# Optimization experiments

Measured on AMD Instinct MI355X. Metric: run time of the kernel, lower is better.

Reference implementation:

```python
import jax, jax.numpy as jnp
import numpy as np

OFFSET_SCALE = 6.0
S = 256
N = S * S  # 65536 UV grid points


def setup_inputs() -> dict:
    key = jax.random.key(0)
    k1, k2, k3, k4 = jax.random.split(key, 4)
    B = 64
    Offset = jax.random.normal(k1, (B, 3, S, S), dtype=jnp.float32)
    Posmap_kpt = jax.random.normal(k2, (B, 3, S, S), dtype=jnp.float32)
    mean_posmap = jax.random.normal(k3, (3, S, S), dtype=jnp.float32)
    uv_kpt = jax.random.randint(k4, (68, 2), 0, S, dtype=jnp.int32)
    return {"Offset": Offset, "Posmap_kpt": Posmap_kpt,
            "mean_posmap": mean_posmap, "uv_kpt": uv_kpt}


def reference(Offset, Posmap_kpt, mean_posmap, uv_kpt):
    B = Offset.shape[0]
    # offsetmap / kptmap: NCHW -> NHWC
    offsetmap = jnp.transpose(Offset * OFFSET_SCALE + mean_posmap[None], (0, 2, 3, 1))  # [B,256,256,3]
    kptmap = jnp.transpose(Posmap_kpt, (0, 2, 3, 1))                                    # [B,256,256,3]

    kpt_dst = kptmap[:, uv_kpt[:, 0], uv_kpt[:, 1]]     # [B,68,3]
    kpt_src = offsetmap[:, uv_kpt[:, 0], uv_kpt[:, 1]]  # [B,68,3]
    offsetflat = offsetmap.reshape(B, N, 3)

    # 16 quadruples of consecutive keypoints: (x, x+1, x+2, x+3) for x in 0,4,...,60
    quad = (jnp.arange(0, 64, 4)[:, None] + jnp.arange(4)[None, :])  # [16,4]
    p = kpt_src[:, quad]  # [B,16,4,3]
    q = kpt_dst[:, quad]  # [B,16,4,3]

    # Batched closed-form rigid fit: A = p0 - p{1,2,3}, Bm = q0 - q{1,2,3}
    A = p[:, :, 0:1, :] - p[:, :, 1:, :]   # [B,16,3,3]
    Bm = q[:, :, 0:1, :] - q[:, :, 1:, :]  # [B,16,3,3]
    R = jnp.linalg.inv(A) @ Bm             # [B,16,3,3]
    T = jnp.mean(q - p @ R, axis=-2)       # [B,16,3]

    # Coarse rotation -> yaw -> keypoint visibility
    R_coarse = jnp.mean(R, axis=1)  # [B,3,3]
    yaw = jnp.arctan2(-R_coarse[:, 2, 0],
                      jnp.sqrt(R_coarse[:, 0, 0] ** 2 + R_coarse[:, 1, 0] ** 2))
    yaw_rate = yaw / jnp.pi
    left = jnp.maximum(yaw_rate * S, 0.0)        # [B]
    right = jnp.minimum(S + yaw_rate * S, float(S))  # [B]
    col = uv_kpt[:, 1].astype(jnp.float32)       # [68]
    vis = jnp.where((col[None, :] <= left[:, None]) | (col[None, :] >= right[:, None]),
                    0.001, 1.0)                  # [B,68]

    # Visibility-weighted average of per-quad transforms
    w = jnp.prod(vis[:, quad], axis=-1)          # [B,16]
    s = jnp.sum(w, axis=1)                       # [B]
    R_p = jnp.einsum('bq,bqij->bij', w, R) / s[:, None, None]  # [B,3,3]
    T_p = jnp.einsum('bq,bqi->bi', w, T) / s[:, None]          # [B,3]

    out = offsetflat @ R_p + T_p[:, None, :]     # [B,65536,3]
    return jnp.transpose(out.reshape(B, S, S, 3), (0, 3, 1, 2))  # [B,3,256,256]
```

## Files before the change

### kernel.cpp

```cpp
#include <hip/hip_runtime.h>
#include <math.h>

#define S 256
#define NPIX (S * S)
#define B 64
#define NQUAD 16

__global__ __launch_bounds__(64) void pose_solve_kernel(
    const float* __restrict__ Offset,
    const float* __restrict__ Posmap,
    const float* __restrict__ meanp,
    const int*   __restrict__ uv,
    float*       __restrict__ params)
{
    const int b = blockIdx.x;
    const int t = threadIdx.x;

    __shared__ double sp[64][3];
    __shared__ double sq[64][3];
    __shared__ double sR[NQUAD][9];
    __shared__ double sT[NQUAD][3];
    __shared__ int    scol[64];

    {
        const int u = uv[2 * t + 0];
        const int v = uv[2 * t + 1];
        scol[t] = v;
        const int n = u * S + v;
        const float* offb = Offset + (size_t)b * 3 * NPIX;
        const float* posb = Posmap + (size_t)b * 3 * NPIX;
#pragma unroll
        for (int c = 0; c < 3; ++c) {
            sp[t][c] = (double)offb[c * NPIX + n] * 6.0 + (double)meanp[c * NPIX + n];
            sq[t][c] = (double)posb[c * NPIX + n];
        }
    }
    __syncthreads();

    if (t < NQUAD) {
        const int k0 = 4 * t;
        double A[3][3], Bm[3][3];
#pragma unroll
        for (int r = 0; r < 3; ++r)
#pragma unroll
            for (int c = 0; c < 3; ++c) {
                A[r][c]  = sp[k0][c] - sp[k0 + 1 + r][c];
                Bm[r][c] = sq[k0][c] - sq[k0 + 1 + r][c];
            }
        const double c00 = A[1][1] * A[2][2] - A[1][2] * A[2][1];
        const double c01 = A[1][2] * A[2][0] - A[1][0] * A[2][2];
        const double c02 = A[1][0] * A[2][1] - A[1][1] * A[2][0];
        const double det = A[0][0] * c00 + A[0][1] * c01 + A[0][2] * c02;
        const double id  = 1.0 / det;
        double inv[3][3];
        inv[0][0] = c00 * id;
        inv[0][1] = (A[0][2] * A[2][1] - A[0][1] * A[2][2]) * id;
        inv[0][2] = (A[0][1] * A[1][2] - A[0][2] * A[1][1]) * id;
        inv[1][0] = c01 * id;
        inv[1][1] = (A[0][0] * A[2][2] - A[0][2] * A[2][0]) * id;
        inv[1][2] = (A[0][2] * A[1][0] - A[0][0] * A[1][2]) * id;
        inv[2][0] = c02 * id;
        inv[2][1] = (A[0][1] * A[2][0] - A[0][0] * A[2][1]) * id;
        inv[2][2] = (A[0][0] * A[1][1] - A[0][1] * A[1][0]) * id;

        double R[3][3];
#pragma unroll
        for (int i = 0; i < 3; ++i)
#pragma unroll
            for (int j = 0; j < 3; ++j) {
                R[i][j] = inv[i][0] * Bm[0][j] + inv[i][1] * Bm[1][j] + inv[i][2] * Bm[2][j];
                sR[t][i * 3 + j] = R[i][j];
            }
#pragma unroll
        for (int c = 0; c < 3; ++c) {
            double acc = 0.0;
#pragma unroll
            for (int j = 0; j < 4; ++j) {
                const double pr = sp[k0 + j][0] * R[0][c] +
                                  sp[k0 + j][1] * R[1][c] +
                                  sp[k0 + j][2] * R[2][c];
                acc += sq[k0 + j][c] - pr;
            }
            sT[t][c] = acc * 0.25;
        }
    }
    __syncthreads();

    if (t == 0) {
        double r00 = 0.0, r10 = 0.0, r20 = 0.0;
        for (int q = 0; q < NQUAD; ++q) {
            r00 += sR[q][0];
            r10 += sR[q][3];
            r20 += sR[q][6];
        }
        r00 /= NQUAD; r10 /= NQUAD; r20 /= NQUAD;
        const double yaw = atan2(-r20, sqrt(r00 * r00 + r10 * r10));
        const double yr  = yaw / M_PI;
        const double left  = fmax(yr * (double)S, 0.0);
        const double right = fmin((double)S + yr * (double)S, (double)S);

        double w[NQUAD];
        double s = 0.0;
        for (int q = 0; q < NQUAD; ++q) {
            double wq = 1.0;
#pragma unroll
            for (int j = 0; j < 4; ++j) {
                const double col = (double)scol[4 * q + j];
                const double vis = (col <= left || col >= right) ? 0.001 : 1.0;
                wq *= vis;
            }
            w[q] = wq;
            s += wq;
        }
        double Rp[9] = {0, 0, 0, 0, 0, 0, 0, 0, 0};
        double Tp[3] = {0, 0, 0};
        for (int q = 0; q < NQUAD; ++q) {
#pragma unroll
            for (int e = 0; e < 9; ++e) Rp[e] += w[q] * sR[q][e];
#pragma unroll
            for (int e = 0; e < 3; ++e) Tp[e] += w[q] * sT[q][e];
        }
        float* pb = params + b * 12;
        const double sinv = 1.0 / s;
#pragma unroll
        for (int e = 0; e < 9; ++e) pb[e] = (float)(Rp[e] * sinv);
#pragma unroll
        for (int e = 0; e < 3; ++e) pb[9 + e] = (float)(Tp[e] * sinv);
    }
}

__global__ __launch_bounds__(256) void apply_pose_kernel(
    const float* __restrict__ Offset,
    const float* __restrict__ meanp,
    const float* __restrict__ params,
    float*       __restrict__ out)
{
    const int tid = blockIdx.x * 256 + threadIdx.x;
    const int b   = tid >> 14;
    const int n   = (tid & 16383) << 2;

    const float* pb = params + b * 12;
    const float r00 = pb[0], r01 = pb[1], r02 = pb[2];
    const float r10 = pb[3], r11 = pb[4], r12 = pb[5];
    const float r20 = pb[6], r21 = pb[7], r22 = pb[8];
    const float t0 = pb[9], t1 = pb[10], t2 = pb[11];

    const float* offb = Offset + (size_t)b * 3 * NPIX;
    const float4 o0 = *(const float4*)(offb + 0 * NPIX + n);
    const float4 o1 = *(const float4*)(offb + 1 * NPIX + n);
    const float4 o2 = *(const float4*)(offb + 2 * NPIX + n);
    const float4 m0 = *(const float4*)(meanp + 0 * NPIX + n);
    const float4 m1 = *(const float4*)(meanp + 1 * NPIX + n);
    const float4 m2 = *(const float4*)(meanp + 2 * NPIX + n);

    float4 x, y, z;
    x.x = fmaf(o0.x, 6.f, m0.x); x.y = fmaf(o0.y, 6.f, m0.y);
    x.z = fmaf(o0.z, 6.f, m0.z); x.w = fmaf(o0.w, 6.f, m0.w);
    y.x = fmaf(o1.x, 6.f, m1.x); y.y = fmaf(o1.y, 6.f, m1.y);
    y.z = fmaf(o1.z, 6.f, m1.z); y.w = fmaf(o1.w, 6.f, m1.w);
    z.x = fmaf(o2.x, 6.f, m2.x); z.y = fmaf(o2.y, 6.f, m2.y);
    z.z = fmaf(o2.z, 6.f, m2.z); z.w = fmaf(o2.w, 6.f, m2.w);

    float4 u, v, wv;
    u.x = fmaf(x.x, r00, fmaf(y.x, r10, fmaf(z.x, r20, t0)));
    u.y = fmaf(x.y, r00, fmaf(y.y, r10, fmaf(z.y, r20, t0)));
    u.z = fmaf(x.z, r00, fmaf(y.z, r10, fmaf(z.z, r20, t0)));
    u.w = fmaf(x.w, r00, fmaf(y.w, r10, fmaf(z.w, r20, t0)));
    v.x = fmaf(x.x, r01, fmaf(y.x, r11, fmaf(z.x, r21, t1)));
    v.y = fmaf(x.y, r01, fmaf(y.y, r11, fmaf(z.y, r21, t1)));
    v.z = fmaf(x.z, r01, fmaf(y.z, r11, fmaf(z.z, r21, t1)));
    v.w = fmaf(x.w, r01, fmaf(y.w, r11, fmaf(z.w, r21, t1)));
    wv.x = fmaf(x.x, r02, fmaf(y.x, r12, fmaf(z.x, r22, t2)));
    wv.y = fmaf(x.y, r02, fmaf(y.y, r12, fmaf(z.y, r22, t2)));
    wv.z = fmaf(x.z, r02, fmaf(y.z, r12, fmaf(z.z, r22, t2)));
    wv.w = fmaf(x.w, r02, fmaf(y.w, r12, fmaf(z.w, r22, t2)));

    float* outb = out + (size_t)b * 3 * NPIX;
    *(float4*)(outb + 0 * NPIX + n) = u;
    *(float4*)(outb + 1 * NPIX + n) = v;
    *(float4*)(outb + 2 * NPIX + n) = wv;
}

extern "C" void kernel_launch(void* const* d_in, const int* in_sizes, int n_in,
                              void* d_out, int out_size, void* d_ws, size_t ws_size,
                              hipStream_t stream) {
    const float* Offset = (const float*)d_in[0];
    const float* Posmap = (const float*)d_in[1];
    const float* meanp  = (const float*)d_in[2];
    const int*   uv     = (const int*)d_in[3];
    float* out = (float*)d_out;
    float* params = (float*)d_ws;

    pose_solve_kernel<<<B, 64, 0, stream>>>(Offset, Posmap, meanp, uv, params);

    const int threads_total = B * (NPIX / 4);
    apply_pose_kernel<<<threads_total / 256, 256, 0, stream>>>(Offset, meanp, params, out);
}
```

Before: 135.9 us.

## Fuse pose solve into apply kernel, recomputing per-block pose redundantly

Merges the two kernels into one: every apply block of 256 threads now gathers the 64 keypoints for its batch, solves the 16 quad rigid fits in double precision, reduces them to a weighted pose in shared memory, then applies it to its own pixels. This removes one kernel launch and the serial dependency between the solve and the apply phases. In exchange, the tiny solve is repeated by all 64 blocks per batch (4096 times instead of 64), including FP64 math and scattered gathers, and adds two block-wide barriers before any output is written. The pixel loads are issued before the solve to hide part of their latency.

After: 220.4 us. +62.2%, slower.

```diff
diff --git a/kernel.cpp b/kernel.cpp
--- a/kernel.cpp
+++ b/kernel.cpp
@@ -6,33 +6,44 @@
 #define B 64
 #define NQUAD 16
 
-__global__ __launch_bounds__(64) void pose_solve_kernel(
+__global__ __launch_bounds__(256) void fused_pose_apply(
     const float* __restrict__ Offset,
     const float* __restrict__ Posmap,
     const float* __restrict__ meanp,
     const int*   __restrict__ uv,
-    float*       __restrict__ params)
+    float*       __restrict__ out)
 {
-    const int b = blockIdx.x;
-    const int t = threadIdx.x;
+    const int tid = blockIdx.x * 256 + threadIdx.x;
+    const int b   = tid >> 14;
+    const int n   = (tid & 16383) << 2;
+    const int t   = threadIdx.x;
 
     __shared__ double sp[64][3];
     __shared__ double sq[64][3];
     __shared__ double sR[NQUAD][9];
     __shared__ double sT[NQUAD][3];
     __shared__ int    scol[64];
+    __shared__ float  sprm[12];
 
-    {
+    const float* offb = Offset + (size_t)b * 3 * NPIX;
+
+    const float4 o0 = *(const float4*)(offb + 0 * NPIX + n);
+    const float4 o1 = *(const float4*)(offb + 1 * NPIX + n);
+    const float4 o2 = *(const float4*)(offb + 2 * NPIX + n);
+    const float4 m0 = *(const float4*)(meanp + 0 * NPIX + n);
+    const float4 m1 = *(const float4*)(meanp + 1 * NPIX + n);
+    const float4 m2 = *(const float4*)(meanp + 2 * NPIX + n);
+
+    if (t < 64) {
         const int u = uv[2 * t + 0];
         const int v = uv[2 * t + 1];
         scol[t] = v;
-        const int n = u * S + v;
-        const float* offb = Offset + (size_t)b * 3 * NPIX;
+        const int kn = u * S + v;
         const float* posb = Posmap + (size_t)b * 3 * NPIX;
 #pragma unroll
         for (int c = 0; c < 3; ++c) {
-            sp[t][c] = (double)offb[c * NPIX + n] * 6.0 + (double)meanp[c * NPIX + n];
-            sq[t][c] = (double)posb[c * NPIX + n];
+            sp[t][c] = (double)offb[c * NPIX + kn] * 6.0 + (double)meanp[c * NPIX + kn];
+            sq[t][c] = (double)posb[c * NPIX + kn];
         }
     }
     __syncthreads();
@@ -120,38 +131,18 @@
 #pragma unroll
             for (int e = 0; e < 3; ++e) Tp[e] += w[q] * sT[q][e];
         }
-        float* pb = params + b * 12;
         const double sinv = 1.0 / s;
 #pragma unroll
-        for (int e = 0; e < 9; ++e) pb[e] = (float)(Rp[e] * sinv);
+        for (int e = 0; e < 9; ++e) sprm[e] = (float)(Rp[e] * sinv);
 #pragma unroll
-        for (int e = 0; e < 3; ++e) pb[9 + e] = (float)(Tp[e] * sinv);
+        for (int e = 0; e < 3; ++e) sprm[9 + e] = (float)(Tp[e] * sinv);
     }
-}
+    __syncthreads();
 
-__global__ __launch_bounds__(256) void apply_pose_kernel(
-    const float* __restrict__ Offset,
-    const float* __restrict__ meanp,
-    const float* __restrict__ params,
-    float*       __restrict__ out)
-{
-    const int tid = blockIdx.x * 256 + threadIdx.x;
-    const int b   = tid >> 14;
-    const int n   = (tid & 16383) << 2;
-
-    const float* pb = params + b * 12;
-    const float r00 = pb[0], r01 = pb[1], r02 = pb[2];
-    const float r10 = pb[3], r11 = pb[4], r12 = pb[5];
-    const float r20 = pb[6], r21 = pb[7], r22 = pb[8];
-    const float t0 = pb[9], t1 = pb[10], t2 = pb[11];
-
-    const float* offb = Offset + (size_t)b * 3 * NPIX;
-    const float4 o0 = *(const float4*)(offb + 0 * NPIX + n);
-    const float4 o1 = *(const float4*)(offb + 1 * NPIX + n);
-    const float4 o2 = *(const float4*)(offb + 2 * NPIX + n);
-    const float4 m0 = *(const float4*)(meanp + 0 * NPIX + n);
-    const float4 m1 = *(const float4*)(meanp + 1 * NPIX + n);
-    const float4 m2 = *(const float4*)(meanp + 2 * NPIX + n);
+    const float r00 = sprm[0], r01 = sprm[1], r02 = sprm[2];
+    const float r10 = sprm[3], r11 = sprm[4], r12 = sprm[5];
+    const float r20 = sprm[6], r21 = sprm[7], r22 = sprm[8];
+    const float t0 = sprm[9], t1 = sprm[10], t2 = sprm[11];
 
     float4 x, y, z;
     x.x = fmaf(o0.x, 6.f, m0.x); x.y = fmaf(o0.y, 6.f, m0.y);
@@ -184,15 +175,14 @@
 extern "C" void kernel_launch(void* const* d_in, const int* in_sizes, int n_in,
                               void* d_out, int out_size, void* d_ws, size_t ws_size,
                               hipStream_t stream) {
+    (void)in_sizes; (void)n_in; (void)out_size; (void)d_ws; (void)ws_size;
     const float* Offset = (const float*)d_in[0];
     const float* Posmap = (const float*)d_in[1];
     const float* meanp  = (const float*)d_in[2];
     const int*   uv     = (const int*)d_in[3];
     float* out = (float*)d_out;
-    float* params = (float*)d_ws;
-
-    pose_solve_kernel<<<B, 64, 0, stream>>>(Offset, Posmap, meanp, uv, params);
 
     const int threads_total = B * (NPIX / 4);
-    apply_pose_kernel<<<threads_total / 256, 256, 0, stream>>>(Offset, meanp, params, out);
+    fused_pose_apply<<<threads_total / 256, 256, 0, stream>>>(
+        Offset, Posmap, meanp, uv, out);
 }
```
